# Optimization experiments

Hardware: AMD Instinct MI355X
Metric: run time of the kernel (lower is better)

## Reference

```python
import jax, jax.numpy as jnp
import numpy as np

EPS = 1e-8  # torch F.cosine_similarity eps

B, H, K = 64, 2048, 256


def setup_inputs() -> dict:
    key = jax.random.key(0)
    k1, k2, k3, k4 = jax.random.split(key, 4)
    input_state = jax.random.normal(k1, (B, H), dtype=jnp.float32)
    knowledge_base = jax.random.normal(k2, (K, B, H), dtype=jnp.float32)
    W = jax.random.normal(k3, (H, H), dtype=jnp.float32) / np.sqrt(H)
    b = jax.random.normal(k4, (H,), dtype=jnp.float32) * 0.02
    return {"input_state": input_state, "knowledge_base": knowledge_base, "W": W, "b": b}


def reference(input_state, knowledge_base, W, b):
    # linear projection (torch Linear: x @ W.T + b)
    q = input_state @ W.T + b                      # [B, H]
    kproj = jnp.einsum('kbh,oh->kbo', knowledge_base, W) + b  # [K, B, H]
    # cosine similarity over last dim, with torch-style eps clamp on norms
    qn = jnp.maximum(jnp.linalg.norm(q, axis=-1), EPS)        # [B]
    kn = jnp.maximum(jnp.linalg.norm(kproj, axis=-1), EPS)    # [K, B]
    dots = jnp.einsum('bh,kbh->kb', q, kproj)                 # [K, B]
    scores = dots / (qn[None, :] * kn)                        # [K, B]
    # softmax over the K knowledge items
    attn = jax.nn.softmax(scores, axis=0)                     # [K, B]
    # output = input + softmax-weighted sum of (raw) knowledge items
    out = input_state + jnp.einsum('kb,kbh->bh', attn, knowledge_base)
    return out
```

## Files before the change

kernel.cpp:

```cpp
#include <hip/hip_runtime.h>
#include <hip/hip_bf16.h>

typedef unsigned short u16;
typedef unsigned int u32;
typedef unsigned long long u64;
typedef __attribute__((ext_vector_type(8))) short short8;
typedef __attribute__((ext_vector_type(4))) float float4v;

#define B_DIM 64
#define H_DIM 2048
#define K_DIM 256
#define NTHR  256

#define WS_WBF   0ull
#define WS_AQ    (8388608ull)
#define WS_Q     (WS_AQ + 524288ull)
#define WS_KN2   (WS_Q + 524288ull)
#define WS_DOTS  (WS_KN2 + 65536ull)
#define WS_KBF   (WS_DOTS + 65536ull)

__device__ __forceinline__ u16 f2bf(float f) {
    unsigned int u = __float_as_uint(f);
    unsigned int r = (u + 0x7fffu + ((u >> 16) & 1u)) >> 16;
    return (u16)r;
}

__device__ __forceinline__ u64 pack4(float4v v) {
    u64 a0 = f2bf(v.x), a1 = f2bf(v.y), a2 = f2bf(v.z), a3 = f2bf(v.w);
    return a0 | (a1 << 16) | (a2 << 32) | (a3 << 48);
}

__device__ __forceinline__ void llds16(const u16* g, const u16* l) {
    __builtin_amdgcn_global_load_lds(
        (__attribute__((address_space(1))) void*)g,
        (__attribute__((address_space(3))) void*)l, 16, 0, 0);
}

__device__ __forceinline__ void gemm0_tile(const u16* __restrict__ Aq, const u16* __restrict__ Wb,
                                           float* __restrict__ qout, u16* As, u16* Bs,
                                           int nt, int ksplit) {
    const int tid = threadIdx.x;
    const int wave = tid >> 6, lane = tid & 63;
    const int l15 = lane & 15, qd = lane >> 4;
    const int wm = wave >> 1, wn = wave & 1;
    const int n0 = nt * 128;
    const int grow = lane >> 2;
    const int gcol = (((lane & 3) ^ ((lane >> 3) & 3)) * 8);
    const int sw = (l15 >> 1) & 3;
    float4v acc[4][4] = {};
    const int kb0 = ksplit * 512;
    for (int kk = 0; kk < 16; ++kk) {
        const int k0 = kb0 + kk * 32;
        #pragma unroll
        for (int i = 0; i < 2; ++i) {
            const int r = wave * 32 + i * 16;
            llds16(Wb + (size_t)(n0 + r + grow) * H_DIM + k0 + gcol, &Bs[r * 32]);
            llds16(Aq + (size_t)(r + grow) * H_DIM + k0 + gcol, &As[r * 32]);
        }
        __syncthreads();
        short8 af[4], bf_[4];
        #pragma unroll
        for (int mi = 0; mi < 4; ++mi)
            af[mi] = *(const short8*)&As[(wm * 64 + mi * 16 + l15) * 32 + ((qd ^ sw) * 8)];
        #pragma unroll
        for (int ni = 0; ni < 4; ++ni)
            bf_[ni] = *(const short8*)&Bs[(wn * 64 + ni * 16 + l15) * 32 + ((qd ^ sw) * 8)];
        #pragma unroll
        for (int mi = 0; mi < 4; ++mi)
            #pragma unroll
            for (int ni = 0; ni < 4; ++ni)
                acc[mi][ni] = __builtin_amdgcn_mfma_f32_16x16x32_bf16(af[mi], bf_[ni], acc[mi][ni], 0, 0, 0);
        __syncthreads();
    }
    const int n0w = n0 + wn * 64;
    if (wm == 0) {
        #pragma unroll
        for (int mi = 0; mi < 4; ++mi)
            #pragma unroll
            for (int reg = 0; reg < 4; ++reg) {
                const int m = mi * 16 + qd * 4 + reg;
                #pragma unroll
                for (int ni = 0; ni < 4; ++ni)
                    atomicAdd(&qout[m * H_DIM + n0w + ni * 16 + l15], acc[mi][ni][reg]);
            }
    }
}

__global__ __launch_bounds__(256) void prep_kernel(
        const float* __restrict__ W, const float* __restrict__ input,
        const float* __restrict__ bias, u16* __restrict__ Wb,
        u16* __restrict__ Aq, float* __restrict__ q,
        float* __restrict__ kn2, float* __restrict__ dots) {
    const int gid = blockIdx.x * NTHR + threadIdx.x;
    ((u64*)Wb)[gid] = pack4(((const float4v*)W)[gid]);
    if (gid < 65536) {
        u64 v = 0;
        if (gid < 32768) v = pack4(((const float4v*)input)[gid]);
        ((u64*)Aq)[gid] = v;
    }
    if (gid < 32768)
        ((float4v*)q)[gid] = ((const float4v*)bias)[gid & 511];
    if (gid < 4096) ((float4v*)kn2)[gid] = float4v{0.f, 0.f, 0.f, 0.f};
    else if (gid < 8192) ((float4v*)dots)[gid - 4096] = float4v{0.f, 0.f, 0.f, 0.f};
}

__global__ __launch_bounds__(256, 4) void mid_kernel(
        const float* __restrict__ kb, const u16* __restrict__ Aq,
        const u16* __restrict__ Wb, float* __restrict__ q, u16* __restrict__ Kbf) {
    __shared__ __align__(16) u16 As[128 * 32];
    __shared__ __align__(16) u16 Bs[128 * 32];
    const int bid = blockIdx.x;
    if (bid < 64) {
        gemm0_tile(Aq, Wb, q, As, Bs, bid & 15, bid >> 4);
    } else {
        const float4v* s4 = (const float4v*)kb;
        u64* d8 = (u64*)Kbf;
        for (int i = (bid - 64) * NTHR + threadIdx.x; i < 8388608; i += 960 * NTHR)
            d8[i] = pack4(s4[i]);
    }
}

#define TILE_BODY(T, bfC, a0C, bfN, a0N)                                        \
  {                                                                             \
    const int t_ = (T);                                                         \
    const u16* As_ = lds + (t_ & 3) * 16384;                                    \
    if (t_ + 3 < 64) stageA(t_ + 3);                                            \
    asm volatile("s_waitcnt lgkmcnt(0)" ::: "memory");                          \
    __builtin_amdgcn_sched_barrier(0);                                          \
    __builtin_amdgcn_s_setprio(1);                                              \
    _Pragma("unroll") for (int mi = 0; mi < 4; ++mi)                            \
      _Pragma("unroll") for (int ni = 0; ni < 4; ++ni)                          \
        acc[mi][ni] = __builtin_amdgcn_mfma_f32_16x16x32_bf16(a0C[mi], bfC[ni], acc[mi][ni], 0, 0, 0); \
    __builtin_amdgcn_s_setprio(0);                                              \
    __builtin_amdgcn_sched_barrier(0);                                          \
    _Pragma("unroll") for (int mi = 0; mi < 4; ++mi)                            \
        a0C[mi] = *(const short8*)&As_[aoff + (4 + mi) * 512];                  \
    if (t_ + 1 < 64) {                                                          \
      const u16* Asn_ = lds + ((t_ + 1) & 3) * 16384;                           \
      const u16* Bsn_ = Asn_ + 8192;                                            \
      _Pragma("unroll") for (int ni = 0; ni < 4; ++ni)                          \
          bfN[ni] = *(const short8*)&Bsn_[boff + ni * 512];                     \
      _Pragma("unroll") for (int mi = 0; mi < 4; ++mi)                          \
          a0N[mi] = *(const short8*)&Asn_[aoff + mi * 512];                     \
    }                                                                           \
    if (t_ + 3 < 64) stageB(t_ + 3);                                            \
    if (t_ + 1 < 64) { asm volatile("s_waitcnt lgkmcnt(8)" ::: "memory"); }     \
    else             { asm volatile("s_waitcnt lgkmcnt(0)" ::: "memory"); }     \
    __builtin_amdgcn_sched_barrier(0);                                          \
    __builtin_amdgcn_s_setprio(1);                                              \
    _Pragma("unroll") for (int mi = 0; mi < 4; ++mi)                            \
      _Pragma("unroll") for (int ni = 0; ni < 4; ++ni)                          \
        acc[4 + mi][ni] = __builtin_amdgcn_mfma_f32_16x16x32_bf16(a0C[mi], bfC[ni], acc[4 + mi][ni], 0, 0, 0); \
    __builtin_amdgcn_s_setprio(0);                                              \
    __builtin_amdgcn_sched_barrier(0);                                          \
    if (t_ <= 60) { asm volatile("s_waitcnt vmcnt(4)" ::: "memory"); }          \
    else          { asm volatile("s_waitcnt vmcnt(0)" ::: "memory"); }          \
    __builtin_amdgcn_s_barrier();                                               \
  }

__global__ __launch_bounds__(512, 2) void gemm_kernel(
        const u16* __restrict__ Kbf, const u16* __restrict__ Wb,
        const float* __restrict__ bias, const float* __restrict__ q,
        float* __restrict__ kn2, float* __restrict__ dots) {
    extern __shared__ __align__(16) u16 lds[];
    const int tid = threadIdx.x;
    const int wave = tid >> 6, lane = tid & 63;
    const int l15 = lane & 15, qd = lane >> 4;
    const int wm = wave >> 2, wn = wave & 3;
    const int nt = blockIdx.x & 7, mt = blockIdx.x >> 3;
    const int m0 = mt * 256, n0 = nt * 256;
    const int grow = wave * 16 + (lane >> 2);
    const int gcol = (((lane & 3) ^ ((lane >> 3) & 3)) * 8);
    const int sw = (l15 >> 1) & 3;

    const u16* srcA = Kbf + (size_t)(m0 + grow) * H_DIM + gcol;
    const u16* srcB = Wb + (size_t)(n0 + grow) * H_DIM + gcol;
    u16* dstBase = lds + wave * 512;

    auto stageA = [&](int t) {
        u16* d = dstBase + (t & 3) * 16384;
        const u16* s = srcA + t * 32;
        llds16(s, d);
        llds16(s + (size_t)128 * H_DIM, d + 4096);
    };
    auto stageB = [&](int t) {
        u16* d = dstBase + (t & 3) * 16384 + 8192;
        const u16* s = srcB + t * 32;
        llds16(s, d);
        llds16(s + (size_t)128 * H_DIM, d + 4096);
    };

    const int aoff = (wm * 128 + l15) * 32 + ((qd ^ sw) * 8);
    const int boff = (wn * 64 + l15) * 32 + ((qd ^ sw) * 8);

    float4v acc[8][4] = {};
    short8 bf0[4], a00[4], bf1[4], a01[4];

    stageA(0); stageB(0); stageA(1); stageB(1); stageA(2); stageB(2);
    asm volatile("s_waitcnt vmcnt(4)" ::: "memory");
    __builtin_amdgcn_sched_barrier(0);
    __builtin_amdgcn_s_barrier();
    {
        const u16* As0 = lds;
        const u16* Bs0 = lds + 8192;
        #pragma unroll
        for (int ni = 0; ni < 4; ++ni) bf0[ni] = *(const short8*)&Bs0[boff + ni * 512];
        #pragma unroll
        for (int mi = 0; mi < 4; ++mi) a00[mi] = *(const short8*)&As0[aoff + mi * 512];
    }

    for (int t = 0; t < 64; t += 2) {
        TILE_BODY(t,     bf0, a00, bf1, a01);
        TILE_BODY(t + 1, bf1, a01, bf0, a00);
    }

    const int n0w = n0 + wn * 64;
    float bv[4];
    #pragma unroll
    for (int ni = 0; ni < 4; ++ni) bv[ni] = bias[n0w + ni * 16 + l15];
    #pragma unroll
    for (int mi = 0; mi < 8; ++mi)
        #pragma unroll
        for (int reg = 0; reg < 4; ++reg) {
            const int mloc = mi * 16 + qd * 4 + reg;
            const int mg = m0 + wm * 128 + mloc;
            const float* qrow = q + (mloc & 63) * H_DIM;
            float s2 = 0.f, sd = 0.f;
            #pragma unroll
            for (int ni = 0; ni < 4; ++ni) {
                const float y = acc[mi][ni][reg] + bv[ni];
                const float qv = qrow[n0w + ni * 16 + l15];
                s2 += y * y; sd += y * qv;
            }
            #pragma unroll
            for (int off = 1; off < 16; off <<= 1) {
                s2 += __shfl_xor(s2, off);
                sd += __shfl_xor(sd, off);
            }
            if (l15 == 0) {
                atomicAdd(&kn2[mg], s2);
                atomicAdd(&dots[mg], sd);
            }
        }
}

__global__ __launch_bounds__(1024) void final_kernel(
        const float* __restrict__ input, const u16* __restrict__ Kbf,
        const float* __restrict__ q, const float* __restrict__ kn2,
        const float* __restrict__ dots, float* __restrict__ out) {
    __shared__ float sm[K_DIM];
    __shared__ float buf[24];
    __shared__ float2 part[1024];
    const int b = blockIdx.x >> 2, hc = blockIdx.x & 3, tid = threadIdx.x;
    const int wave = tid >> 6, lane = tid & 63;
    float s = 0.f;
    #pragma unroll
    for (int i = 0; i < 2; ++i) {
        float v = q[b * H_DIM + i * 1024 + tid];
        s += v * v;
    }
    #pragma unroll
    for (int o = 32; o >= 1; o >>= 1) s += __shfl_xor(s, o);
    if (lane == 0) buf[wave] = s;
    __syncthreads();
    float qs = 0.f;
    #pragma unroll
    for (int i = 0; i < 16; ++i) qs += buf[i];
    const float qn = fmaxf(sqrtf(qs), 1e-8f);
    __syncthreads();
    float sc = 0.f;
    if (tid < K_DIM) {
        const float kn = fmaxf(sqrtf(kn2[tid * B_DIM + b]), 1e-8f);
        sc = dots[tid * B_DIM + b] / (qn * kn);
        float mx = sc;
        #pragma unroll
        for (int o = 32; o >= 1; o >>= 1) mx = fmaxf(mx, __shfl_xor(mx, o));
        if (lane == 0) buf[16 + wave] = mx;
    }
    __syncthreads();
    const float mx = fmaxf(fmaxf(buf[16], buf[17]), fmaxf(buf[18], buf[19]));
    __syncthreads();
    if (tid < K_DIM) {
        const float e = expf(sc - mx);
        float se = e;
        #pragma unroll
        for (int o = 32; o >= 1; o >>= 1) se += __shfl_xor(se, o);
        if (lane == 0) buf[20 + wave] = se;
        sm[tid] = e;
    }
    __syncthreads();
    const float sei = 1.f / (buf[20] + buf[21] + buf[22] + buf[23]);
    __syncthreads();
    const int col = tid & 255, quarter = tid >> 8;
    const int h2 = hc * 256 + col;
    const u32* basep = (const u32*)Kbf + ((size_t)(quarter * 64 * B_DIM + b)) * (H_DIM / 2) + h2;
    const float* smq = sm + quarter * 64;
    float s0 = 0.f, s1 = 0.f;
    #pragma unroll 8
    for (int i = 0; i < 64; ++i) {
        const u32 p = basep[(size_t)i * (B_DIM * H_DIM / 2)];
        const float a = smq[i];
        s0 += a * __uint_as_float(p << 16);
        s1 += a * __uint_as_float(p & 0xffff0000u);
    }
    part[tid] = float2{s0, s1};
    __syncthreads();
    if (tid < 256) {
        float2 p0 = part[tid], p1 = part[256 + tid], p2 = part[512 + tid], p3 = part[768 + tid];
        const int h = h2 * 2;
        float2 iv = *(const float2*)&input[(size_t)b * H_DIM + h];
        float2 r;
        r.x = iv.x + (p0.x + p1.x + p2.x + p3.x) * sei;
        r.y = iv.y + (p0.y + p1.y + p2.y + p3.y) * sei;
        *(float2*)&out[(size_t)b * H_DIM + h] = r;
    }
}

extern "C" void kernel_launch(void* const* d_in, const int* in_sizes, int n_in,
                              void* d_out, int out_size, void* d_ws, size_t ws_size,
                              hipStream_t stream) {
    const float* input = (const float*)d_in[0];
    const float* kb    = (const float*)d_in[1];
    const float* W     = (const float*)d_in[2];
    const float* bias  = (const float*)d_in[3];
    float* out = (float*)d_out;
    char* ws = (char*)d_ws;

    u16*   Wb   = (u16*)(ws + WS_WBF);
    u16*   Aq   = (u16*)(ws + WS_AQ);
    float* q    = (float*)(ws + WS_Q);
    float* kn2  = (float*)(ws + WS_KN2);
    float* dots = (float*)(ws + WS_DOTS);
    u16*   Kbf  = (u16*)(ws + WS_KBF);

    static int lds_set = 0;
    if (!lds_set) {
        hipFuncSetAttribute((const void*)gemm_kernel,
                            hipFuncAttributeMaxDynamicSharedMemorySize, 131072);
        lds_set = 1;
    }

    prep_kernel<<<4096, NTHR, 0, stream>>>(W, input, bias, Wb, Aq, q, kn2, dots);
    mid_kernel<<<1024, NTHR, 0, stream>>>(kb, Aq, Wb, q, Kbf);
    gemm_kernel<<<512, 512, 131072, stream>>>(Kbf, Wb, bias, q, kn2, dots);
    final_kernel<<<256, 1024, 0, stream>>>(input, Kbf, q, kn2, dots, out);
}
```

Before: 367.1 us.

## Pre-tile bf16 operands into swizzled contiguous layout and reduce epilogue atomics via LDS

The conversion passes for W and the knowledge base now write bf16 data in a tiled, pre-swizzled layout, so each 32-wide K-slice of a 256-row tile is contiguous. The GEMM staging loads then read long linear runs instead of strided rows. The GEMM epilogue first reduces the per-wave norm and dot partials in LDS and issues one atomic per row per block instead of one per wave. The final kernel now reads the original fp32 knowledge base instead of the bf16 copy, which doubles the bytes read in that pass but avoids rounding error in the weighted sum.

```diff
diff --git a/kernel.cpp b/kernel.cpp
--- a/kernel.cpp
+++ b/kernel.cpp
@@ -19,6 +19,7 @@
 #define WS_DOTS  (WS_KN2 + 65536ull)
 #define WS_KBF   (WS_DOTS + 65536ull)
 
+
 __device__ __forceinline__ u16 f2bf(float f) {
     unsigned int u = __float_as_uint(f);
     unsigned int r = (u + 0x7fffu + ((u >> 16) & 1u)) >> 16;
@@ -34,6 +35,19 @@
     __builtin_amdgcn_global_load_lds(
         (__attribute__((address_space(1))) void*)g,
         (__attribute__((address_space(3))) void*)l, 16, 0, 0);
+}
+
+__device__ __forceinline__ void tile_granule(const float* __restrict__ src,
+                                             u64* __restrict__ dst, int go) {
+    const int p   = go >> 17;
+    const int rem = go & 131071;
+    const int t   = rem >> 11;
+    const int rr  = rem & 2047;
+    const int r   = rr >> 3;
+    const int gg  = rr & 7;
+    const int gs  = (((gg >> 1) ^ ((r >> 1) & 3)) << 3) + ((gg & 1) << 2);
+    const float4v v = *(const float4v*)&src[((size_t)(p * 256 + r)) * H_DIM + t * 32 + gs];
+    dst[go] = pack4(v);
 }
 
 __device__ __forceinline__ void gemm0_tile(const u16* __restrict__ Aq, const u16* __restrict__ Wb,
@@ -47,14 +61,17 @@
     const int grow = lane >> 2;
     const int gcol = (((lane & 3) ^ ((lane >> 3) & 3)) * 8);
     const int sw = (l15 >> 1) & 3;
+    const u16* wbase = Wb + (size_t)(nt >> 1) * 524288 + (size_t)((nt & 1) * 128) * 32
+                          + (size_t)lane * 8;
     float4v acc[4][4] = {};
     const int kb0 = ksplit * 512;
     for (int kk = 0; kk < 16; ++kk) {
         const int k0 = kb0 + kk * 32;
+        const int t = ksplit * 16 + kk;
         #pragma unroll
         for (int i = 0; i < 2; ++i) {
             const int r = wave * 32 + i * 16;
-            llds16(Wb + (size_t)(n0 + r + grow) * H_DIM + k0 + gcol, &Bs[r * 32]);
+            llds16(wbase + (size_t)t * 8192 + (size_t)r * 32, &Bs[r * 32]);
             llds16(Aq + (size_t)(r + grow) * H_DIM + k0 + gcol, &As[r * 32]);
         }
         __syncthreads();
@@ -92,7 +109,7 @@
         u16* __restrict__ Aq, float* __restrict__ q,
         float* __restrict__ kn2, float* __restrict__ dots) {
     const int gid = blockIdx.x * NTHR + threadIdx.x;
-    ((u64*)Wb)[gid] = pack4(((const float4v*)W)[gid]);
+    tile_granule(W, (u64*)Wb, gid);
     if (gid < 65536) {
         u64 v = 0;
         if (gid < 32768) v = pack4(((const float4v*)input)[gid]);
@@ -113,10 +130,9 @@
     if (bid < 64) {
         gemm0_tile(Aq, Wb, q, As, Bs, bid & 15, bid >> 4);
     } else {
-        const float4v* s4 = (const float4v*)kb;
         u64* d8 = (u64*)Kbf;
-        for (int i = (bid - 64) * NTHR + threadIdx.x; i < 8388608; i += 960 * NTHR)
-            d8[i] = pack4(s4[i]);
+        for (int go = (bid - 64) * NTHR + threadIdx.x; go < 8388608; go += 960 * NTHR)
+            tile_granule(kb, d8, go);
     }
 }
 
@@ -169,25 +185,23 @@
     const int wm = wave >> 2, wn = wave & 3;
     const int nt = blockIdx.x & 7, mt = blockIdx.x >> 3;
     const int m0 = mt * 256, n0 = nt * 256;
-    const int grow = wave * 16 + (lane >> 2);
-    const int gcol = (((lane & 3) ^ ((lane >> 3) & 3)) * 8);
     const int sw = (l15 >> 1) & 3;
 
-    const u16* srcA = Kbf + (size_t)(m0 + grow) * H_DIM + gcol;
-    const u16* srcB = Wb + (size_t)(n0 + grow) * H_DIM + gcol;
+    const u16* srcA = Kbf + (size_t)mt * 524288 + wave * 512 + lane * 8;
+    const u16* srcB = Wb  + (size_t)nt * 524288 + wave * 512 + lane * 8;
     u16* dstBase = lds + wave * 512;
 
     auto stageA = [&](int t) {
         u16* d = dstBase + (t & 3) * 16384;
-        const u16* s = srcA + t * 32;
+        const u16* s = srcA + (size_t)t * 8192;
         llds16(s, d);
-        llds16(s + (size_t)128 * H_DIM, d + 4096);
+        llds16(s + 4096, d + 4096);
     };
     auto stageB = [&](int t) {
         u16* d = dstBase + (t & 3) * 16384 + 8192;
-        const u16* s = srcB + t * 32;
+        const u16* s = srcB + (size_t)t * 8192;
         llds16(s, d);
-        llds16(s + (size_t)128 * H_DIM, d + 4096);
+        llds16(s + 4096, d + 4096);
     };
 
     const int aoff = (wm * 128 + l15) * 32 + ((qd ^ sw) * 8);
@@ -215,6 +229,7 @@
     }
 
     const int n0w = n0 + wn * 64;
+    float* red = (float*)lds;
     float bv[4];
     #pragma unroll
     for (int ni = 0; ni < 4; ++ni) bv[ni] = bias[n0w + ni * 16 + l15];
@@ -223,7 +238,6 @@
         #pragma unroll
         for (int reg = 0; reg < 4; ++reg) {
             const int mloc = mi * 16 + qd * 4 + reg;
-            const int mg = m0 + wm * 128 + mloc;
             const float* qrow = q + (mloc & 63) * H_DIM;
             float s2 = 0.f, sd = 0.f;
             #pragma unroll
@@ -238,14 +252,22 @@
                 sd += __shfl_xor(sd, off);
             }
             if (l15 == 0) {
-                atomicAdd(&kn2[mg], s2);
-                atomicAdd(&dots[mg], sd);
+                const int row = wm * 128 + mloc;
+                red[wn * 256 + row] = s2;
+                red[1024 + wn * 256 + row] = sd;
             }
         }
+    __syncthreads();
+    if (tid < 256) {
+        const float k2 = red[tid] + red[256 + tid] + red[512 + tid] + red[768 + tid];
+        const float dd = red[1024 + tid] + red[1280 + tid] + red[1536 + tid] + red[1792 + tid];
+        atomicAdd(&kn2[m0 + tid], k2);
+        atomicAdd(&dots[m0 + tid], dd);
+    }
 }
 
 __global__ __launch_bounds__(1024) void final_kernel(
-        const float* __restrict__ input, const u16* __restrict__ Kbf,
+        const float* __restrict__ input, const float* __restrict__ kb,
         const float* __restrict__ q, const float* __restrict__ kn2,
         const float* __restrict__ dots, float* __restrict__ out) {
     __shared__ float sm[K_DIM];
@@ -293,15 +315,16 @@
     __syncthreads();
     const int col = tid & 255, quarter = tid >> 8;
     const int h2 = hc * 256 + col;
-    const u32* basep = (const u32*)Kbf + ((size_t)(quarter * 64 * B_DIM + b)) * (H_DIM / 2) + h2;
+    const float2* basep = (const float2*)kb
+        + ((size_t)(quarter * 64 * B_DIM + b)) * (H_DIM / 2) + h2;
     const float* smq = sm + quarter * 64;
     float s0 = 0.f, s1 = 0.f;
     #pragma unroll 8
     for (int i = 0; i < 64; ++i) {
-        const u32 p = basep[(size_t)i * (B_DIM * H_DIM / 2)];
+        const float2 p = basep[(size_t)i * (B_DIM * H_DIM / 2)];
         const float a = smq[i];
-        s0 += a * __uint_as_float(p << 16);
-        s1 += a * __uint_as_float(p & 0xffff0000u);
+        s0 += a * p.x;
+        s1 += a * p.y;
     }
     part[tid] = float2{s0, s1};
     __syncthreads();
@@ -343,5 +366,5 @@
     prep_kernel<<<4096, NTHR, 0, stream>>>(W, input, bias, Wb, Aq, q, kn2, dots);
     mid_kernel<<<1024, NTHR, 0, stream>>>(kb, Aq, Wb, q, Kbf);
     gemm_kernel<<<512, 512, 131072, stream>>>(Kbf, Wb, bias, q, kn2, dots);
-    final_kernel<<<256, 1024, 0, stream>>>(input, Kbf, q, kn2, dots, out);
-}
+    final_kernel<<<256, 1024, 0, stream>>>(input, kb, q, kn2, dots, out);
+}
```

Result: no change. 362.1 us (-1.4%).
